# Optimization experiments

Hardware: AMD Instinct MI355X
Metric: run time of the kernel (lower is better)

The kernel has to match this reference:

```python
import jax, jax.numpy as jnp
import numpy as np

B, N, DIN, DOUT, H = 4, 2048, 256, 256, 4
HD = DOUT // H
NEG_SLOPE = 0.2


def setup_inputs() -> dict:
    key = jax.random.key(0)
    k1, k2, k3, k4, k5 = jax.random.split(key, 5)
    x = jax.random.normal(k1, (B, N, DIN), dtype=jnp.float32)
    adj = jax.random.randint(k2, (B, N, N), 0, 2).astype(jnp.float32)
    # ensure self-loops so every softmax row has at least one valid entry
    adj = jnp.maximum(adj, jnp.eye(N, dtype=jnp.float32)[None])
    # xavier-uniform-ish scales
    w_bound = float(np.sqrt(6.0 / (DIN + DOUT)))
    a_bound = float(np.sqrt(6.0 / (1 + HD)))
    W = jax.random.uniform(k3, (DOUT, DIN), jnp.float32, -w_bound, w_bound)
    a_src = jax.random.uniform(k4, (H, HD), jnp.float32, -a_bound, a_bound)
    a_dst = jax.random.uniform(k5, (H, HD), jnp.float32, -a_bound, a_bound)
    return {"x": x, "adj": adj, "W": W, "a_src": a_src, "a_dst": a_dst}


def reference(x, adj, W, a_src, a_dst):
    b, n, _ = x.shape
    h = (x @ W.T).reshape(b, n, H, HD)                      # [B,N,H,HD]
    s_src = jnp.einsum('bnhd,hd->bnh', h, a_src)            # [B,N,H]
    s_dst = jnp.einsum('bnhd,hd->bnh', h, a_dst)            # [B,N,H]
    # e[b,i,j,h] = leaky_relu(s_src[b,i,h] + s_dst[b,j,h])
    e = jax.nn.leaky_relu(s_src[:, :, None, :] + s_dst[:, None, :, :], NEG_SLOPE)
    e = jnp.where(adj[..., None] == 0, -jnp.inf, e)         # [B,N,N,H]
    alpha = jax.nn.softmax(e, axis=2)                       # softmax over j (dropout is identity at eval)
    out = jnp.einsum('bijh,bjhd->bihd', alpha, h)           # weighted aggregate
    return out.reshape(b, n, DOUT)
```

## Files before the change

kernel.cpp:

```cpp
#include <hip/hip_runtime.h>
#include <math.h>

#define Bb   4
#define Nn   2048
#define Dd   256
#define Hh   4
#define HDd  64
#define BN   (Bb * Nn)

typedef float v4f __attribute__((ext_vector_type(4)));
typedef short v8s __attribute__((ext_vector_type(8)));

__device__ __forceinline__ unsigned rne_bf16(float f) {
    unsigned u = __float_as_uint(f);
    u += 0x7fffu + ((u >> 16) & 1u);
    return u >> 16;
}

__global__ __launch_bounds__(256, 2) void k_gemm(const float* __restrict__ x,
                                                 const float* __restrict__ W,
                                                 const float* __restrict__ a_src,
                                                 const float* __restrict__ a_dst,
                                                 const float* __restrict__ adj,
                                                 unsigned short* __restrict__ hbf,
                                                 float* __restrict__ ssrc,
                                                 float* __restrict__ sdst,
                                                 unsigned long long* __restrict__ bitadj) {
    __shared__ __align__(16) unsigned short xs[2][64 * 72];
    __shared__ __align__(16) unsigned short wsm[2][64 * 72];
    __shared__ float asd[128];

    if (blockIdx.x >= 512) {
        const int gw = ((int)blockIdx.x - 512) * 4 + ((int)threadIdx.x >> 6);
        const int lane = (int)threadIdx.x & 63;
#pragma unroll 1
        for (int w = gw * 4; w < 262144; w += 8192 * 4) {
            float v0 = adj[(size_t)((w + 0) >> 5) * 2048 + ((w + 0) & 31) * 64 + lane];
            float v1 = adj[(size_t)((w + 1) >> 5) * 2048 + ((w + 1) & 31) * 64 + lane];
            float v2 = adj[(size_t)((w + 2) >> 5) * 2048 + ((w + 2) & 31) * 64 + lane];
            float v3 = adj[(size_t)((w + 3) >> 5) * 2048 + ((w + 3) & 31) * 64 + lane];
            unsigned long long m0 = __ballot(v0 != 0.0f);
            unsigned long long m1 = __ballot(v1 != 0.0f);
            unsigned long long m2 = __ballot(v2 != 0.0f);
            unsigned long long m3 = __ballot(v3 != 0.0f);
            if (lane == 0) {
                bitadj[w + 0] = m0;
                bitadj[w + 1] = m1;
                bitadj[w + 2] = m2;
                bitadj[w + 3] = m3;
            }
        }
        return;
    }

    const int tid = threadIdx.x;
    const int m0 = (int)(blockIdx.x >> 2) * 64;
    const int head = (int)blockIdx.x & 3;
    const int n0 = head * 64;
    const int b = m0 >> 11;
    const int i0loc = m0 & 2047;

    if (tid < 128) {
        int sel = tid >> 6, d = tid & 63;
        asd[tid] = sel ? a_dst[n0 + d] : a_src[n0 + d];
    }

    const int wv = tid >> 6, ln = tid & 63, l15 = ln & 15, l4 = ln >> 4;
    const int mh = wv >> 1, nh = wv & 1;
    const int srow = tid >> 2, kq = (tid & 3) * 16;

    v4f acc[2][2];
#pragma unroll
    for (int g = 0; g < 2; ++g)
#pragma unroll
        for (int t = 0; t < 2; ++t) acc[g][t] = (v4f){0.f, 0.f, 0.f, 0.f};

    for (int st = 0; st < 4; ++st) {
        const int k0 = st * 64;
        __syncthreads();
        {
            float xf[16], wf[16];
            const float* xp = x + (size_t)(m0 + srow) * Dd + k0 + kq;
            const float* wp = W + (size_t)(n0 + srow) * Dd + k0 + kq;
#pragma unroll
            for (int q = 0; q < 4; ++q) {
                *(float4*)&xf[q * 4] = *(const float4*)(xp + q * 4);
                *(float4*)&wf[q * 4] = *(const float4*)(wp + q * 4);
            }
            unsigned xh[8], xl[8], wh[8], wl[8];
#pragma unroll
            for (int j = 0; j < 8; ++j) {
                unsigned h0 = rne_bf16(xf[2 * j]), h1 = rne_bf16(xf[2 * j + 1]);
                float l0 = xf[2 * j] - __uint_as_float(h0 << 16);
                float l1 = xf[2 * j + 1] - __uint_as_float(h1 << 16);
                xh[j] = h0 | (h1 << 16);
                xl[j] = rne_bf16(l0) | (rne_bf16(l1) << 16);
                unsigned g0 = rne_bf16(wf[2 * j]), g1 = rne_bf16(wf[2 * j + 1]);
                float m0f = wf[2 * j] - __uint_as_float(g0 << 16);
                float m1f = wf[2 * j + 1] - __uint_as_float(g1 << 16);
                wh[j] = g0 | (g1 << 16);
                wl[j] = rne_bf16(m0f) | (rne_bf16(m1f) << 16);
            }
            *(uint4*)(xs[0] + srow * 72 + kq)     = make_uint4(xh[0], xh[1], xh[2], xh[3]);
            *(uint4*)(xs[0] + srow * 72 + kq + 8) = make_uint4(xh[4], xh[5], xh[6], xh[7]);
            *(uint4*)(xs[1] + srow * 72 + kq)     = make_uint4(xl[0], xl[1], xl[2], xl[3]);
            *(uint4*)(xs[1] + srow * 72 + kq + 8) = make_uint4(xl[4], xl[5], xl[6], xl[7]);
            *(uint4*)(wsm[0] + srow * 72 + kq)     = make_uint4(wh[0], wh[1], wh[2], wh[3]);
            *(uint4*)(wsm[0] + srow * 72 + kq + 8) = make_uint4(wh[4], wh[5], wh[6], wh[7]);
            *(uint4*)(wsm[1] + srow * 72 + kq)     = make_uint4(wl[0], wl[1], wl[2], wl[3]);
            *(uint4*)(wsm[1] + srow * 72 + kq + 8) = make_uint4(wl[4], wl[5], wl[6], wl[7]);
        }
        __syncthreads();
        {
            v8s ah[2][2], al[2][2], bh_[2][2], bl_[2][2];
#pragma unroll
            for (int g = 0; g < 2; ++g)
#pragma unroll
                for (int kh = 0; kh < 2; ++kh) {
                    int ro = (mh * 32 + g * 16 + l15) * 72 + kh * 32 + l4 * 8;
                    ah[g][kh] = *(const v8s*)(xs[0] + ro);
                    al[g][kh] = *(const v8s*)(xs[1] + ro);
                }
#pragma unroll
            for (int t = 0; t < 2; ++t)
#pragma unroll
                for (int kh = 0; kh < 2; ++kh) {
                    int ro = (nh * 32 + t * 16 + l15) * 72 + kh * 32 + l4 * 8;
                    bh_[t][kh] = *(const v8s*)(wsm[0] + ro);
                    bl_[t][kh] = *(const v8s*)(wsm[1] + ro);
                }
#pragma unroll
            for (int g = 0; g < 2; ++g)
#pragma unroll
                for (int t = 0; t < 2; ++t)
#pragma unroll
                    for (int kh = 0; kh < 2; ++kh) {
                        acc[g][t] = __builtin_amdgcn_mfma_f32_16x16x32_bf16(ah[g][kh], bh_[t][kh], acc[g][t], 0, 0, 0);
                        acc[g][t] = __builtin_amdgcn_mfma_f32_16x16x32_bf16(al[g][kh], bh_[t][kh], acc[g][t], 0, 0, 0);
                        acc[g][t] = __builtin_amdgcn_mfma_f32_16x16x32_bf16(ah[g][kh], bl_[t][kh], acc[g][t], 0, 0, 0);
                    }
        }
    }

    __syncthreads();
    float* T = (float*)&xs[0][0];
#pragma unroll
    for (int g = 0; g < 2; ++g)
#pragma unroll
        for (int t = 0; t < 2; ++t)
#pragma unroll
            for (int r = 0; r < 4; ++r) {
                int d = nh * 32 + t * 16 + l15;
                int m = mh * 32 + g * 16 + l4 * 4 + r;
                T[d * 67 + m] = acc[g][t][r];
            }
    __syncthreads();
    if (tid < 128) {
        int m = tid & 63, sel = tid >> 6;
        float s = 0.f;
#pragma unroll
        for (int d = 0; d < 64; ++d) s += T[d * 67 + m] * asd[sel * 64 + d];
        (sel ? sdst : ssrc)[(size_t)head * BN + (size_t)b * Nn + i0loc + m] = s;
        int dloc = tid >> 1, jh = tid & 1;
        const float* row = T + dloc * 67 + jh * 32;
        unsigned pk[16];
#pragma unroll
        for (int jj = 0; jj < 16; ++jj)
            pk[jj] = rne_bf16(row[jj * 2]) | (rne_bf16(row[jj * 2 + 1]) << 16);
        unsigned short* dst = hbf +
            ((size_t)((b * 64 + (i0loc >> 5) + jh) * 256 + head * HDd + dloc)) * 32;
        uint4* d4 = (uint4*)dst;
        d4[0] = make_uint4(pk[0], pk[1], pk[2], pk[3]);
        d4[1] = make_uint4(pk[4], pk[5], pk[6], pk[7]);
        d4[2] = make_uint4(pk[8], pk[9], pk[10], pk[11]);
        d4[3] = make_uint4(pk[12], pk[13], pk[14], pk[15]);
    }
}

__global__ __launch_bounds__(512, 4) void k_aggr(const unsigned short* __restrict__ hbf,
                                                 const unsigned long long* __restrict__ bitadj,
                                                 const float* __restrict__ ssrc,
                                                 const float* __restrict__ sdst,
                                                 float* __restrict__ out) {
    __shared__ __align__(16) float sdl[4 * 2048];
    __shared__ __align__(16) float red[4 * 64 * 20];

    const int tid = threadIdx.x;
    const int bid = (int)blockIdx.x;
    const int b  = bid >> 7;
    const int i0 = (bid & 127) * 16;

    const int wv = tid >> 6;
    const int h  = wv & 3;
    const int jh = wv >> 2;
    const int ln = tid & 63, l15 = ln & 15, l4 = ln >> 4;

    for (int q = tid; q < 2048; q += 512) {
        int hh = q >> 9, j = (q & 511) * 4;
        *(float4*)&sdl[hh * 2048 + j] =
            *(const float4*)(sdst + (size_t)hh * BN + (size_t)b * Nn + j);
    }

    const int irow = i0 + l15;
    const float ss = ssrc[(size_t)h * BN + (size_t)b * Nn + irow];
    const unsigned char* ajr = (const unsigned char*)bitadj +
        ((size_t)b * Nn + irow) * 256 + jh * 128;
    const unsigned short* hb0 = hbf +
        ((size_t)b * 64 * 256 + (size_t)(h * HDd + l15)) * 32 + l4 * 8;
    const float* sdb = sdl + h * 2048 + jh * 1024 + l4 * 8;
    const unsigned mbase = 1u << (l4 * 8);

    const v8s ones = {0x3F80, 0x3F80, 0x3F80, 0x3F80, 0x3F80, 0x3F80, 0x3F80, 0x3F80};

    v4f acc0 = (v4f){0.f, 0.f, 0.f, 0.f}, acc1 = acc0, acc2 = acc0, acc3 = acc0, zac = acc0;
    v8s bb0, bb1, bb2, bb3, bb4, bb5, bb6, bb7;
    uint2 ajA, ajB;

    __syncthreads();

#define LOADB(S_) do {                                                        \
        const unsigned short* hq_ = hb0 + (size_t)(jh * 16 + (S_)) * 16384;   \
        bb0 = *(const v8s*)(hq_ + 0);                                         \
        bb1 = *(const v8s*)(hq_ + 8192);                                      \
        bb2 = *(const v8s*)(hq_ + 512);                                       \
        bb3 = *(const v8s*)(hq_ + 8192 + 512);                                \
        bb4 = *(const v8s*)(hq_ + 1024);                                      \
        bb5 = *(const v8s*)(hq_ + 8192 + 1024);                               \
        bb6 = *(const v8s*)(hq_ + 1536);                                      \
        bb7 = *(const v8s*)(hq_ + 8192 + 1536);                               \
    } while (0)

#define LOADADJ(S_, A_) do {                                                  \
        A_ = *(const uint2*)(ajr + ((S_) & 15) * 8);                          \
    } while (0)

#define GENP(sdv) ({                                                          \
        float e_ = ss + (sdv);                                                \
        e_ = fmaxf(e_, 0.2f * e_);                                            \
        __expf(e_);                                                           \
    })

#define SEL(W_, K_, P_) (((W_) & (mbase << (K_))) ? (P_) : 0.0f)

#define GENFRAG(dst, W_, sdx, sdy) do {                                       \
        float p0_ = GENP(sdx.x), p1_ = GENP(sdx.y);                           \
        float p2_ = GENP(sdx.z), p3_ = GENP(sdx.w);                           \
        float p4_ = GENP(sdy.x), p5_ = GENP(sdy.y);                           \
        float p6_ = GENP(sdy.z), p7_ = GENP(sdy.w);                           \
        float w0_ = SEL(W_, 0, p0_), w1_ = SEL(W_, 1, p1_);                   \
        float w2_ = SEL(W_, 2, p2_), w3_ = SEL(W_, 3, p3_);                   \
        float w4_ = SEL(W_, 4, p4_), w5_ = SEL(W_, 5, p5_);                   \
        float w6_ = SEL(W_, 6, p6_), w7_ = SEL(W_, 7, p7_);                   \
        union { v8s v; unsigned u[4]; } P_;                                   \
        P_.u[0] = rne_bf16(w0_) | (rne_bf16(w1_) << 16);                      \
        P_.u[1] = rne_bf16(w2_) | (rne_bf16(w3_) << 16);                      \
        P_.u[2] = rne_bf16(w4_) | (rne_bf16(w5_) << 16);                      \
        P_.u[3] = rne_bf16(w6_) | (rne_bf16(w7_) << 16);                      \
        dst = P_.v;                                                           \
    } while (0)

#define STEPX(S_, AJ_) do {                                                   \
        const float* sdp_ = sdb + (S_) * 64;                                  \
        const float4 sd0_ = *(const float4*)(sdp_);                           \
        const float4 sd1_ = *(const float4*)(sdp_ + 4);                       \
        const float4 sd2_ = *(const float4*)(sdp_ + 32);                      \
        const float4 sd3_ = *(const float4*)(sdp_ + 36);                      \
        v8s afr0_, afr1_;                                                     \
        GENFRAG(afr0_, AJ_.x, sd0_, sd1_);                                    \
        GENFRAG(afr1_, AJ_.y, sd2_, sd3_);                                    \
        acc0 = __builtin_amdgcn_mfma_f32_16x16x32_bf16(afr0_, bb0, acc0, 0, 0, 0); \
        acc1 = __builtin_amdgcn_mfma_f32_16x16x32_bf16(afr0_, bb2, acc1, 0, 0, 0); \
        acc2 = __builtin_amdgcn_mfma_f32_16x16x32_bf16(afr0_, bb4, acc2, 0, 0, 0); \
        acc3 = __builtin_amdgcn_mfma_f32_16x16x32_bf16(afr0_, bb6, acc3, 0, 0, 0); \
        zac  = __builtin_amdgcn_mfma_f32_16x16x32_bf16(afr0_, ones, zac, 0, 0, 0); \
        acc0 = __builtin_amdgcn_mfma_f32_16x16x32_bf16(afr1_, bb1, acc0, 0, 0, 0); \
        acc1 = __builtin_amdgcn_mfma_f32_16x16x32_bf16(afr1_, bb3, acc1, 0, 0, 0); \
        acc2 = __builtin_amdgcn_mfma_f32_16x16x32_bf16(afr1_, bb5, acc2, 0, 0, 0); \
        acc3 = __builtin_amdgcn_mfma_f32_16x16x32_bf16(afr1_, bb7, acc3, 0, 0, 0); \
        zac  = __builtin_amdgcn_mfma_f32_16x16x32_bf16(afr1_, ones, zac, 0, 0, 0); \
    } while (0)

    LOADADJ(0, ajA);
#pragma unroll 1
    for (int s = 0; s < 16; s += 2) {
        LOADB(s);
        LOADADJ(s + 1, ajB);
        __builtin_amdgcn_sched_barrier(0);
        STEPX(s, ajA);
        LOADB(s + 1);
        LOADADJ(s + 2, ajA);
        __builtin_amdgcn_sched_barrier(0);
        STEPX(s + 1, ajB);
    }

#undef LOADB
#undef LOADADJ
#undef GENP
#undef SEL
#undef GENFRAG
#undef STEPX

    float* rp = red + (h * 64 + ln) * 20;
    if (jh) {
        *(v4f*)(rp + 0)  = acc0;
        *(v4f*)(rp + 4)  = acc1;
        *(v4f*)(rp + 8)  = acc2;
        *(v4f*)(rp + 12) = acc3;
        *(v4f*)(rp + 16) = zac;
    }
    __syncthreads();
    if (!jh) {
        acc0 += *(const v4f*)(rp + 0);
        acc1 += *(const v4f*)(rp + 4);
        acc2 += *(const v4f*)(rp + 8);
        acc3 += *(const v4f*)(rp + 12);
        zac  += *(const v4f*)(rp + 16);
        float zi[4];
#pragma unroll
        for (int r = 0; r < 4; ++r) zi[r] = 1.f / zac[r];
        float* op = out + ((size_t)b * Nn + i0 + l4 * 4) * Dd + h * HDd + l15;
#pragma unroll
        for (int r = 0; r < 4; ++r) {
            op[(size_t)r * Dd + 0]  = acc0[r] * zi[r];
            op[(size_t)r * Dd + 16] = acc1[r] * zi[r];
            op[(size_t)r * Dd + 32] = acc2[r] * zi[r];
            op[(size_t)r * Dd + 48] = acc3[r] * zi[r];
        }
    }
}

extern "C" void kernel_launch(void* const* d_in, const int* in_sizes, int n_in,
                              void* d_out, int out_size, void* d_ws, size_t ws_size,
                              hipStream_t stream) {
    const float* x     = (const float*)d_in[0];
    const float* adj   = (const float*)d_in[1];
    const float* W     = (const float*)d_in[2];
    const float* a_src = (const float*)d_in[3];
    const float* a_dst = (const float*)d_in[4];
    float* out = (float*)d_out;

    unsigned short* hbf = (unsigned short*)d_ws;
    float* ssrc = (float*)(hbf + (size_t)Bb * Nn * Dd);
    float* sdst = ssrc + (size_t)Hh * BN;
    unsigned long long* bitadj = (unsigned long long*)(sdst + (size_t)Hh * BN);

    k_gemm<<<dim3(2560), dim3(256), 0, stream>>>(x, W, a_src, a_dst, adj,
                                                 hbf, ssrc, sdst, bitadj);
    k_aggr<<<dim3(512), dim3(512), 0, stream>>>(hbf, bitadj, ssrc, sdst, out);
}
```

Measured before the change: 154.6 us.

## Factor leaky-relu exponentials into precomputed tables and rebalance block mapping

```diff
diff --git a/kernel.cpp b/kernel.cpp
--- a/kernel.cpp
+++ b/kernel.cpp
@@ -30,11 +30,12 @@
     __shared__ __align__(16) unsigned short wsm[2][64 * 72];
     __shared__ float asd[128];
 
-    if (blockIdx.x >= 512) {
-        const int gw = ((int)blockIdx.x - 512) * 4 + ((int)threadIdx.x >> 6);
+    const int bid0 = (int)blockIdx.x;
+    if (bid0 & 1) {
+        const int gw = (bid0 >> 1) * 4 + ((int)threadIdx.x >> 6);
         const int lane = (int)threadIdx.x & 63;
 #pragma unroll 1
-        for (int w = gw * 4; w < 262144; w += 8192 * 4) {
+        for (int w = gw * 4; w < 262144; w += 2048 * 4) {
             float v0 = adj[(size_t)((w + 0) >> 5) * 2048 + ((w + 0) & 31) * 64 + lane];
             float v1 = adj[(size_t)((w + 1) >> 5) * 2048 + ((w + 1) & 31) * 64 + lane];
             float v2 = adj[(size_t)((w + 2) >> 5) * 2048 + ((w + 2) & 31) * 64 + lane];
@@ -53,9 +54,11 @@
         return;
     }
 
+    const int g = bid0 >> 1;
+    const int head = (g >> 2) & 3;
+    const int mtile = (g & 3) + 4 * (g >> 4);
     const int tid = threadIdx.x;
-    const int m0 = (int)(blockIdx.x >> 2) * 64;
-    const int head = (int)blockIdx.x & 3;
+    const int m0 = mtile * 64;
     const int n0 = head * 64;
     const int b = m0 >> 11;
     const int i0loc = m0 & 2047;
@@ -71,9 +74,9 @@
 
     v4f acc[2][2];
 #pragma unroll
-    for (int g = 0; g < 2; ++g)
-#pragma unroll
-        for (int t = 0; t < 2; ++t) acc[g][t] = (v4f){0.f, 0.f, 0.f, 0.f};
+    for (int gg = 0; gg < 2; ++gg)
+#pragma unroll
+        for (int t = 0; t < 2; ++t) acc[gg][t] = (v4f){0.f, 0.f, 0.f, 0.f};
 
     for (int st = 0; st < 4; ++st) {
         const int k0 = st * 64;
@@ -114,12 +117,12 @@
         {
             v8s ah[2][2], al[2][2], bh_[2][2], bl_[2][2];
 #pragma unroll
-            for (int g = 0; g < 2; ++g)
+            for (int gg = 0; gg < 2; ++gg)
 #pragma unroll
                 for (int kh = 0; kh < 2; ++kh) {
-                    int ro = (mh * 32 + g * 16 + l15) * 72 + kh * 32 + l4 * 8;
-                    ah[g][kh] = *(const v8s*)(xs[0] + ro);
-                    al[g][kh] = *(const v8s*)(xs[1] + ro);
+                    int ro = (mh * 32 + gg * 16 + l15) * 72 + kh * 32 + l4 * 8;
+                    ah[gg][kh] = *(const v8s*)(xs[0] + ro);
+                    al[gg][kh] = *(const v8s*)(xs[1] + ro);
                 }
 #pragma unroll
             for (int t = 0; t < 2; ++t)
@@ -130,14 +133,14 @@
                     bl_[t][kh] = *(const v8s*)(wsm[1] + ro);
                 }
 #pragma unroll
-            for (int g = 0; g < 2; ++g)
+            for (int gg = 0; gg < 2; ++gg)
 #pragma unroll
                 for (int t = 0; t < 2; ++t)
 #pragma unroll
                     for (int kh = 0; kh < 2; ++kh) {
-                        acc[g][t] = __builtin_amdgcn_mfma_f32_16x16x32_bf16(ah[g][kh], bh_[t][kh], acc[g][t], 0, 0, 0);
-                        acc[g][t] = __builtin_amdgcn_mfma_f32_16x16x32_bf16(al[g][kh], bh_[t][kh], acc[g][t], 0, 0, 0);
-                        acc[g][t] = __builtin_amdgcn_mfma_f32_16x16x32_bf16(ah[g][kh], bl_[t][kh], acc[g][t], 0, 0, 0);
+                        acc[gg][t] = __builtin_amdgcn_mfma_f32_16x16x32_bf16(ah[gg][kh], bh_[t][kh], acc[gg][t], 0, 0, 0);
+                        acc[gg][t] = __builtin_amdgcn_mfma_f32_16x16x32_bf16(al[gg][kh], bh_[t][kh], acc[gg][t], 0, 0, 0);
+                        acc[gg][t] = __builtin_amdgcn_mfma_f32_16x16x32_bf16(ah[gg][kh], bl_[t][kh], acc[gg][t], 0, 0, 0);
                     }
         }
     }
@@ -145,14 +148,14 @@
     __syncthreads();
     float* T = (float*)&xs[0][0];
 #pragma unroll
-    for (int g = 0; g < 2; ++g)
+    for (int gg = 0; gg < 2; ++gg)
 #pragma unroll
         for (int t = 0; t < 2; ++t)
 #pragma unroll
             for (int r = 0; r < 4; ++r) {
                 int d = nh * 32 + t * 16 + l15;
-                int m = mh * 32 + g * 16 + l4 * 4 + r;
-                T[d * 67 + m] = acc[g][t][r];
+                int m = mh * 32 + gg * 16 + l4 * 4 + r;
+                T[d * 67 + m] = acc[gg][t][r];
             }
     __syncthreads();
     if (tid < 128) {
@@ -161,14 +164,14 @@
 #pragma unroll
         for (int d = 0; d < 64; ++d) s += T[d * 67 + m] * asd[sel * 64 + d];
         (sel ? sdst : ssrc)[(size_t)head * BN + (size_t)b * Nn + i0loc + m] = s;
-        int dloc = tid >> 1, jh = tid & 1;
-        const float* row = T + dloc * 67 + jh * 32;
+        int dloc = tid >> 1, jhh = tid & 1;
+        const float* row = T + dloc * 67 + jhh * 32;
         unsigned pk[16];
 #pragma unroll
         for (int jj = 0; jj < 16; ++jj)
             pk[jj] = rne_bf16(row[jj * 2]) | (rne_bf16(row[jj * 2 + 1]) << 16);
         unsigned short* dst = hbf +
-            ((size_t)((b * 64 + (i0loc >> 5) + jh) * 256 + head * HDd + dloc)) * 32;
+            ((size_t)((b * 64 + (i0loc >> 5) + jhh) * 256 + head * HDd + dloc)) * 32;
         uint4* d4 = (uint4*)dst;
         d4[0] = make_uint4(pk[0], pk[1], pk[2], pk[3]);
         d4[1] = make_uint4(pk[4], pk[5], pk[6], pk[7]);
@@ -182,13 +185,13 @@
                                                  const float* __restrict__ ssrc,
                                                  const float* __restrict__ sdst,
                                                  float* __restrict__ out) {
-    __shared__ __align__(16) float sdl[4 * 2048];
-    __shared__ __align__(16) float red[4 * 64 * 20];
+    __shared__ __align__(16) float dtab[4 * 2048 * 2];
 
     const int tid = threadIdx.x;
     const int bid = (int)blockIdx.x;
-    const int b  = bid >> 7;
-    const int i0 = (bid & 127) * 16;
+    const int xcd = bid & 7;
+    const int b   = xcd >> 1;
+    const int i0  = (((bid >> 3) << 1) | (xcd & 1)) * 16;
 
     const int wv = tid >> 6;
     const int h  = wv & 3;
@@ -196,110 +199,110 @@
     const int ln = tid & 63, l15 = ln & 15, l4 = ln >> 4;
 
     for (int q = tid; q < 2048; q += 512) {
-        int hh = q >> 9, j = (q & 511) * 4;
-        *(float4*)&sdl[hh * 2048 + j] =
-            *(const float4*)(sdst + (size_t)hh * BN + (size_t)b * Nn + j);
+        int hh = q >> 9, j4 = (q & 511) * 4;
+        float4 sv = *(const float4*)(sdst + (size_t)hh * BN + (size_t)b * Nn + j4);
+        float4 o0 = make_float4(__expf(sv.x), __expf(0.2f * sv.x),
+                                __expf(sv.y), __expf(0.2f * sv.y));
+        float4 o1 = make_float4(__expf(sv.z), __expf(0.2f * sv.z),
+                                __expf(sv.w), __expf(0.2f * sv.w));
+        *(float4*)&dtab[(hh * 2048 + j4) * 2]     = o0;
+        *(float4*)&dtab[(hh * 2048 + j4) * 2 + 4] = o1;
     }
 
     const int irow = i0 + l15;
     const float ss = ssrc[(size_t)h * BN + (size_t)b * Nn + irow];
+    const float c1 = __expf(ss), c2 = __expf(0.2f * ss);
     const unsigned char* ajr = (const unsigned char*)bitadj +
         ((size_t)b * Nn + irow) * 256 + jh * 128;
     const unsigned short* hb0 = hbf +
         ((size_t)b * 64 * 256 + (size_t)(h * HDd + l15)) * 32 + l4 * 8;
-    const float* sdb = sdl + h * 2048 + jh * 1024 + l4 * 8;
-    const unsigned mbase = 1u << (l4 * 8);
+    const float* dtb = dtab + (h * 2048 + jh * 1024 + l4 * 8) * 2;
 
     const v8s ones = {0x3F80, 0x3F80, 0x3F80, 0x3F80, 0x3F80, 0x3F80, 0x3F80, 0x3F80};
 
     v4f acc0 = (v4f){0.f, 0.f, 0.f, 0.f}, acc1 = acc0, acc2 = acc0, acc3 = acc0, zac = acc0;
-    v8s bb0, bb1, bb2, bb3, bb4, bb5, bb6, bb7;
-    uint2 ajA, ajB;
-
-    __syncthreads();
-
-#define LOADB(S_) do {                                                        \
-        const unsigned short* hq_ = hb0 + (size_t)(jh * 16 + (S_)) * 16384;   \
-        bb0 = *(const v8s*)(hq_ + 0);                                         \
-        bb1 = *(const v8s*)(hq_ + 8192);                                      \
-        bb2 = *(const v8s*)(hq_ + 512);                                       \
-        bb3 = *(const v8s*)(hq_ + 8192 + 512);                                \
-        bb4 = *(const v8s*)(hq_ + 1024);                                      \
-        bb5 = *(const v8s*)(hq_ + 8192 + 1024);                               \
-        bb6 = *(const v8s*)(hq_ + 1536);                                      \
-        bb7 = *(const v8s*)(hq_ + 8192 + 1536);                               \
+    v8s bbA[8], bbB[8];
+    unsigned mA0, mB0, mA1, mB1;
+
+    __syncthreads();
+
+#define LOADB(S_, BB) do {                                                    \
+        const unsigned short* hq_ = hb0 +                                     \
+            (size_t)((jh * 16 + ((S_) & 15)) * 16384);                        \
+        BB[0] = *(const v8s*)(hq_ + 0);                                       \
+        BB[1] = *(const v8s*)(hq_ + 8192);                                    \
+        BB[2] = *(const v8s*)(hq_ + 512);                                     \
+        BB[3] = *(const v8s*)(hq_ + 8192 + 512);                              \
+        BB[4] = *(const v8s*)(hq_ + 1024);                                    \
+        BB[5] = *(const v8s*)(hq_ + 8192 + 1024);                             \
+        BB[6] = *(const v8s*)(hq_ + 1536);                                    \
+        BB[7] = *(const v8s*)(hq_ + 8192 + 1536);                             \
     } while (0)
 
-#define LOADADJ(S_, A_) do {                                                  \
-        A_ = *(const uint2*)(ajr + ((S_) & 15) * 8);                          \
+#define LOADADJ(S_, MA_, MB_) do {                                            \
+        MA_ = ajr[((S_) & 15) * 8 + l4];                                      \
+        MB_ = ajr[((S_) & 15) * 8 + 4 + l4];                                  \
     } while (0)
 
-#define GENP(sdv) ({                                                          \
-        float e_ = ss + (sdv);                                                \
-        e_ = fmaxf(e_, 0.2f * e_);                                            \
-        __expf(e_);                                                           \
-    })
-
-#define SEL(W_, K_, P_) (((W_) & (mbase << (K_))) ? (P_) : 0.0f)
-
-#define GENFRAG(dst, W_, sdx, sdy) do {                                       \
-        float p0_ = GENP(sdx.x), p1_ = GENP(sdx.y);                           \
-        float p2_ = GENP(sdx.z), p3_ = GENP(sdx.w);                           \
-        float p4_ = GENP(sdy.x), p5_ = GENP(sdy.y);                           \
-        float p6_ = GENP(sdy.z), p7_ = GENP(sdy.w);                           \
-        float w0_ = SEL(W_, 0, p0_), w1_ = SEL(W_, 1, p1_);                   \
-        float w2_ = SEL(W_, 2, p2_), w3_ = SEL(W_, 3, p3_);                   \
-        float w4_ = SEL(W_, 4, p4_), w5_ = SEL(W_, 5, p5_);                   \
-        float w6_ = SEL(W_, 6, p6_), w7_ = SEL(W_, 7, p7_);                   \
+#define GENFRAG(dst, M_, dd_) do {                                            \
+        const float4 q0_ = *(const float4*)((dd_) + 0);                       \
+        const float4 q1_ = *(const float4*)((dd_) + 4);                       \
+        const float4 q2_ = *(const float4*)((dd_) + 8);                       \
+        const float4 q3_ = *(const float4*)((dd_) + 12);                      \
+        float w0_ = ((M_) & 1u)   ? fmaxf(c1 * q0_.x, c2 * q0_.y) : 0.f;      \
+        float w1_ = ((M_) & 2u)   ? fmaxf(c1 * q0_.z, c2 * q0_.w) : 0.f;      \
+        float w2_ = ((M_) & 4u)   ? fmaxf(c1 * q1_.x, c2 * q1_.y) : 0.f;      \
+        float w3_ = ((M_) & 8u)   ? fmaxf(c1 * q1_.z, c2 * q1_.w) : 0.f;      \
+        float w4_ = ((M_) & 16u)  ? fmaxf(c1 * q2_.x, c2 * q2_.y) : 0.f;      \
+        float w5_ = ((M_) & 32u)  ? fmaxf(c1 * q2_.z, c2 * q2_.w) : 0.f;      \
+        float w6_ = ((M_) & 64u)  ? fmaxf(c1 * q3_.x, c2 * q3_.y) : 0.f;      \
+        float w7_ = ((M_) & 128u) ? fmaxf(c1 * q3_.z, c2 * q3_.w) : 0.f;      \
         union { v8s v; unsigned u[4]; } P_;                                   \
-        P_.u[0] = rne_bf16(w0_) | (rne_bf16(w1_) << 16);                      \
-        P_.u[1] = rne_bf16(w2_) | (rne_bf16(w3_) << 16);                      \
-        P_.u[2] = rne_bf16(w4_) | (rne_bf16(w5_) << 16);                      \
-        P_.u[3] = rne_bf16(w6_) | (rne_bf16(w7_) << 16);                      \
+        asm("v_cvt_pk_bf16_f32 %0, %1, %2" : "=v"(P_.u[0]) : "v"(w0_), "v"(w1_)); \
+        asm("v_cvt_pk_bf16_f32 %0, %1, %2" : "=v"(P_.u[1]) : "v"(w2_), "v"(w3_)); \
+        asm("v_cvt_pk_bf16_f32 %0, %1, %2" : "=v"(P_.u[2]) : "v"(w4_), "v"(w5_)); \
+        asm("v_cvt_pk_bf16_f32 %0, %1, %2" : "=v"(P_.u[3]) : "v"(w6_), "v"(w7_)); \
         dst = P_.v;                                                           \
     } while (0)
 
-#define STEPX(S_, AJ_) do {                                                   \
-        const float* sdp_ = sdb + (S_) * 64;                                  \
-        const float4 sd0_ = *(const float4*)(sdp_);                           \
-        const float4 sd1_ = *(const float4*)(sdp_ + 4);                       \
-        const float4 sd2_ = *(const float4*)(sdp_ + 32);                      \
-        const float4 sd3_ = *(const float4*)(sdp_ + 36);                      \
+#define STEPX(S_, BB, MA_, MB_) do {                                          \
+        const float* dd_ = dtb + (S_) * 128;                                  \
         v8s afr0_, afr1_;                                                     \
-        GENFRAG(afr0_, AJ_.x, sd0_, sd1_);                                    \
-        GENFRAG(afr1_, AJ_.y, sd2_, sd3_);                                    \
-        acc0 = __builtin_amdgcn_mfma_f32_16x16x32_bf16(afr0_, bb0, acc0, 0, 0, 0); \
-        acc1 = __builtin_amdgcn_mfma_f32_16x16x32_bf16(afr0_, bb2, acc1, 0, 0, 0); \
-        acc2 = __builtin_amdgcn_mfma_f32_16x16x32_bf16(afr0_, bb4, acc2, 0, 0, 0); \
-        acc3 = __builtin_amdgcn_mfma_f32_16x16x32_bf16(afr0_, bb6, acc3, 0, 0, 0); \
-        zac  = __builtin_amdgcn_mfma_f32_16x16x32_bf16(afr0_, ones, zac, 0, 0, 0); \
-        acc0 = __builtin_amdgcn_mfma_f32_16x16x32_bf16(afr1_, bb1, acc0, 0, 0, 0); \
-        acc1 = __builtin_amdgcn_mfma_f32_16x16x32_bf16(afr1_, bb3, acc1, 0, 0, 0); \
-        acc2 = __builtin_amdgcn_mfma_f32_16x16x32_bf16(afr1_, bb5, acc2, 0, 0, 0); \
-        acc3 = __builtin_amdgcn_mfma_f32_16x16x32_bf16(afr1_, bb7, acc3, 0, 0, 0); \
-        zac  = __builtin_amdgcn_mfma_f32_16x16x32_bf16(afr1_, ones, zac, 0, 0, 0); \
+        GENFRAG(afr0_, MA_, dd_);                                             \
+        GENFRAG(afr1_, MB_, dd_ + 64);                                        \
+        acc0 = __builtin_amdgcn_mfma_f32_16x16x32_bf16(afr0_, BB[0], acc0, 0, 0, 0); \
+        acc1 = __builtin_amdgcn_mfma_f32_16x16x32_bf16(afr0_, BB[2], acc1, 0, 0, 0); \
+        acc2 = __builtin_amdgcn_mfma_f32_16x16x32_bf16(afr0_, BB[4], acc2, 0, 0, 0); \
+        acc3 = __builtin_amdgcn_mfma_f32_16x16x32_bf16(afr0_, BB[6], acc3, 0, 0, 0); \
+        zac  = __builtin_amdgcn_mfma_f32_16x16x32_bf16(afr0_, ones,  zac,  0, 0, 0); \
+        acc0 = __builtin_amdgcn_mfma_f32_16x16x32_bf16(afr1_, BB[1], acc0, 0, 0, 0); \
+        acc1 = __builtin_amdgcn_mfma_f32_16x16x32_bf16(afr1_, BB[3], acc1, 0, 0, 0); \
+        acc2 = __builtin_amdgcn_mfma_f32_16x16x32_bf16(afr1_, BB[5], acc2, 0, 0, 0); \
+        acc3 = __builtin_amdgcn_mfma_f32_16x16x32_bf16(afr1_, BB[7], acc3, 0, 0, 0); \
+        zac  = __builtin_amdgcn_mfma_f32_16x16x32_bf16(afr1_, ones,  zac,  0, 0, 0); \
     } while (0)
 
-    LOADADJ(0, ajA);
+    LOADB(0, bbA);
+    LOADADJ(0, mA0, mB0);
 #pragma unroll 1
     for (int s = 0; s < 16; s += 2) {
-        LOADB(s);
-        LOADADJ(s + 1, ajB);
+        LOADB(s + 1, bbB);
+        LOADADJ(s + 1, mA1, mB1);
         __builtin_amdgcn_sched_barrier(0);
-        STEPX(s, ajA);
-        LOADB(s + 1);
-        LOADADJ(s + 2, ajA);
+        STEPX(s, bbA, mA0, mB0);
+        LOADB(s + 2, bbA);
+        LOADADJ(s + 2, mA0, mB0);
         __builtin_amdgcn_sched_barrier(0);
-        STEPX(s + 1, ajB);
+        STEPX(s + 1, bbB, mA1, mB1);
     }
 
 #undef LOADB
 #undef LOADADJ
-#undef GENP
-#undef SEL
 #undef GENFRAG
 #undef STEPX
 
+    __syncthreads();
+    float* red = dtab;
     float* rp = red + (h * 64 + ln) * 20;
     if (jh) {
         *(v4f*)(rp + 0)  = acc0;
@@ -344,7 +347,7 @@
     float* sdst = ssrc + (size_t)Hh * BN;
     unsigned long long* bitadj = (unsigned long long*)(sdst + (size_t)Hh * BN);
 
-    k_gemm<<<dim3(2560), dim3(256), 0, stream>>>(x, W, a_src, a_dst, adj,
+    k_gemm<<<dim3(1024), dim3(256), 0, stream>>>(x, W, a_src, a_dst, adj,
                                                  hbf, ssrc, sdst, bitadj);
     k_aggr<<<dim3(512), dim3(512), 0, stream>>>(hbf, bitadj, ssrc, sdst, out);
 }
```

Result: slower. 168.9 us (+9.3%).
